# Performance work log

Measured on AMD Instinct MI355X. Metric: run time of the kernel, lower is better.

Reference implementation:

```python
import jax, jax.numpy as jnp
import numpy as np
import math

D_MODEL = 1024
D_HEAD = 64
BATCH = 8
SEQ = 2048


def setup_inputs() -> dict:
    key = jax.random.key(0)
    ks = jax.random.split(key, 5)
    s = 0.02
    return {
        "residual_stream": jax.random.normal(ks[0], (BATCH, SEQ, D_MODEL), dtype=jnp.float32),
        "Wq": jax.random.normal(ks[1], (D_HEAD, D_MODEL), dtype=jnp.float32) * s,
        "Wk": jax.random.normal(ks[2], (D_HEAD, D_MODEL), dtype=jnp.float32) * s,
        "Wv": jax.random.normal(ks[3], (D_HEAD, D_MODEL), dtype=jnp.float32) * s,
        "Wo": jax.random.normal(ks[4], (D_MODEL, D_HEAD), dtype=jnp.float32) * s,
    }


def reference(residual_stream, Wq, Wk, Wv, Wo):
    # NOTE: module scales by 1/sqrt(d_model), NOT 1/sqrt(d_head)
    scale = 1.0 / math.sqrt(D_MODEL)
    q = jnp.einsum('bsd,hd->bsh', residual_stream, Wq)  # [B,S,Dh]
    k = jnp.einsum('bsd,hd->bsh', residual_stream, Wk)  # [B,S,Dh]
    scores = jnp.einsum('bqh,bkh->bqk', q, k) * scale   # [B,S,S]
    seq = scores.shape[-1]
    causal = jnp.tril(jnp.ones((seq, seq), dtype=bool))
    scores = jnp.where(causal[None, :, :], scores, jnp.float32(-jnp.inf))
    attn = jax.nn.softmax(scores, axis=-1)
    # O applied to V *before* the attention-weighted sum (as in the module)
    x = jnp.einsum('bsh,dh->bsd', jnp.einsum('bsd,hd->bsh', residual_stream, Wv), Wo)  # [B,S,Dm]
    return jnp.einsum('bqk,bkd->bqd', attn, x)
```

## Files before the change

kernel.cpp:

```cpp
#include <hip/hip_runtime.h>

#define SEQ 2048
#define DMODEL 1024
#define DHEAD 64
#define NROWS 16384
#define ATT_SC2 0.0450842300667f

typedef __attribute__((ext_vector_type(8))) short bf16x8;
typedef __attribute__((ext_vector_type(4))) float f32x4;
typedef __attribute__((ext_vector_type(4))) unsigned int u32x4;
typedef __attribute__((ext_vector_type(4))) unsigned short u16x4;
typedef __attribute__((ext_vector_type(4))) float fl4;

#define MFMA16(a,b,c) __builtin_amdgcn_mfma_f32_16x16x32_bf16((a),(b),(c),0,0,0)
#define GLL16(g, l) __builtin_amdgcn_global_load_lds( \
    (const __attribute__((address_space(1))) void*)(g), \
    (__attribute__((address_space(3))) void*)(l), 16, 0, 0)

__device__ __forceinline__ unsigned short f2bf(float f) {
    union { float f; unsigned int u; } v; v.f = f;
    unsigned int u = v.u;
    unsigned int r = u + 0x7fffu + ((u >> 16) & 1u);
    return (unsigned short)(r >> 16);
}

__device__ __forceinline__ unsigned int cvtpk(float lo, float hi) {
    unsigned int d;
    asm volatile("v_cvt_pk_bf16_f32 %0, %1, %2" : "=v"(d) : "v"(lo), "v"(hi));
    return d;
}

__global__ __launch_bounds__(256) void k_cvt(
    const float* __restrict__ Wq, const float* __restrict__ Wk,
    const float* __restrict__ Wv, const float* __restrict__ Wo,
    unsigned short* __restrict__ Wb,
    unsigned short* __restrict__ Wob)
{
    int i4 = blockIdx.x * 256 + threadIdx.x;
    const int W1 = 16384;
    const float* src; unsigned short* dst; int off;
    if (i4 < 3 * W1) {
        int which = i4 / W1;
        off = i4 - which * W1;
        src = (which == 0) ? Wq : (which == 1) ? Wk : Wv;
        dst = Wb + (size_t)which * 65536;
    } else {
        off = i4 - 3 * W1; src = Wo; dst = Wob;
    }
    fl4 v = reinterpret_cast<const fl4*>(src)[off];
    u16x4 o;
    o[0] = f2bf(v[0]); o[1] = f2bf(v[1]); o[2] = f2bf(v[2]); o[3] = f2bf(v[3]);
    reinterpret_cast<u16x4*>(dst)[off] = o;
}

__global__ __launch_bounds__(256) void k_qkv(
    const float* __restrict__ x,
    const unsigned short* __restrict__ Wb,
    unsigned short* __restrict__ Qb,
    unsigned short* __restrict__ Kb,
    unsigned short* __restrict__ Vt)
{
    __shared__ __align__(16) char smem[65536];

    int tid = threadIdx.x;
    int wave = tid >> 6, lane = tid & 63, g = lane >> 4, lr = lane & 15;
    int mh = wave & 1, nh = wave >> 1;
    int mbase = blockIdx.x * 32;

    const float* xsrc[2];
#pragma unroll
    for (int j = 0; j < 2; ++j) {
        int ci = j * 256 + tid;
        int row = ci >> 4, c = ci & 15, cg = c ^ (row & 7);
        xsrc[j] = x + (size_t)(mbase + row) * DMODEL + cg * 4;
    }
    const unsigned short* wsrc[6];
#pragma unroll
    for (int j = 0; j < 6; ++j) {
        int ci = (wave * 6 + j) * 64 + lane;
        int row = ci >> 3, c = ci & 7, cg = c ^ (row & 7);
        wsrc[j] = Wb + (size_t)row * DMODEL + cg * 8;
    }

    f32x4 acc[6];
#pragma unroll
    for (int f = 0; f < 6; ++f) acc[f] = (f32x4){0.f, 0.f, 0.f, 0.f};

#pragma unroll
    for (int j = 0; j < 2; ++j) GLL16(xsrc[j], smem + j * 4096 + wave * 1024);
#pragma unroll
    for (int j = 0; j < 6; ++j) GLL16(wsrc[j], smem + 16384 + (wave * 6 + j) * 1024);

    for (int ks = 0; ks < 16; ++ks) {
        int cur = ks & 1;
        if (ks < 15) {
            int nb = cur ^ 1;
#pragma unroll
            for (int j = 0; j < 2; ++j)
                GLL16(xsrc[j] + (ks + 1) * 64, smem + nb * 8192 + j * 4096 + wave * 1024);
#pragma unroll
            for (int j = 0; j < 6; ++j)
                GLL16(wsrc[j] + (ks + 1) * 64,
                      smem + 16384 + nb * 24576 + (wave * 6 + j) * 1024);
            asm volatile("s_waitcnt vmcnt(8)" ::: "memory");
        } else {
            asm volatile("s_waitcnt vmcnt(0)" ::: "memory");
        }
        __builtin_amdgcn_s_barrier();
        asm volatile("" ::: "memory");

        const float* Xf = (const float*)(smem + cur * 8192);
        const unsigned short* Wf = (const unsigned short*)(smem + 16384 + cur * 24576);
        int arow = mh * 16 + lr;
#pragma unroll
        for (int kc = 0; kc < 2; ++kc) {
            int c0 = (kc * 8 + g * 2) ^ (lr & 7);
            int c1 = (kc * 8 + g * 2 + 1) ^ (lr & 7);
            fl4 xa = *(const fl4*)&Xf[arow * 64 + c0 * 4];
            fl4 xb = *(const fl4*)&Xf[arow * 64 + c1 * 4];
            union { unsigned int u[4]; bf16x8 v; } a;
            a.u[0] = cvtpk(xa[0], xa[1]); a.u[1] = cvtpk(xa[2], xa[3]);
            a.u[2] = cvtpk(xb[0], xb[1]); a.u[3] = cvtpk(xb[2], xb[3]);
            __builtin_amdgcn_s_setprio(1);
#pragma unroll
            for (int f = 0; f < 6; ++f) {
                int brow = (nh * 6 + f) * 16 + lr;
                int cb = (kc * 4 + g) ^ (lr & 7);
                bf16x8 b = *(const bf16x8*)&Wf[brow * 64 + cb * 8];
                acc[f] = MFMA16(a.v, b, acc[f]);
            }
            __builtin_amdgcn_s_setprio(0);
        }
        asm volatile("" ::: "memory");
        __builtin_amdgcn_s_barrier();
    }

    unsigned short* tmp = (unsigned short*)smem;
    int mrow = mbase + mh * 16 + g * 4;
#pragma unroll
    for (int f = 0; f < 6; ++f) {
        int fg = nh * 6 + f;
#pragma unroll
        for (int r = 0; r < 4; ++r) {
            unsigned short bv = f2bf(acc[f][r]);
            if (fg < 4)      Qb[(size_t)(mrow + r) * DHEAD + fg * 16 + lr] = bv;
            else if (fg < 8) Kb[(size_t)(mrow + r) * DHEAD + (fg - 4) * 16 + lr] = bv;
            else             tmp[(mh * 16 + g * 4 + r) * 72 + (fg - 8) * 16 + lr] = bv;
        }
    }
    __syncthreads();
    int b = mbase >> 11, sbase = mbase & 2047;
    int h = tid >> 2, sc = tid & 3;
    u32x4 o;
#pragma unroll
    for (int j = 0; j < 4; ++j) {
        o[j] = (unsigned int)tmp[(sc * 8 + 2 * j) * 72 + h] |
               ((unsigned int)tmp[(sc * 8 + 2 * j + 1) * 72 + h] << 16);
    }
    size_t off = ((size_t)(b * 64 + h)) * SEQ + sbase + sc * 8;
    *reinterpret_cast<u32x4*>(&Vt[off]) = o;
}

__global__ __launch_bounds__(256) void k_fused(
    const unsigned short* __restrict__ Qb,
    const unsigned short* __restrict__ Kb,
    const unsigned short* __restrict__ Vt,
    const unsigned short* __restrict__ Wob,
    float* __restrict__ out)
{
    __shared__ __align__(16) char smem[65536];

    int tid = threadIdx.x;
    int wave = tid >> 6, lane = tid & 63, g = lane >> 4, lr = lane & 15;
    int pair = wave >> 1, pw = wave & 1;
    int bid = blockIdx.x;
    int idx = bid & 255;
    int qt = (bid < 256) ? (63 - (idx >> 3)) : (idx >> 3);
    int b = idx & 7;

    const unsigned short* ksrc[2];
    const unsigned short* vsrc[2];
#pragma unroll
    for (int j = 0; j < 2; ++j) {
        int ci = j * 256 + tid;
        int row = ci >> 3, c = ci & 7, cg = c ^ (row & 7);
        ksrc[j] = Kb + ((size_t)(b * SEQ) + row) * DHEAD + cg * 8;
        vsrc[j] = Vt + ((size_t)(b * DHEAD) + row) * SEQ + cg * 8;
    }

#define STAGE(n_, s_) do {                                                   \
    int te_ = (2 * (s_)) * 64;                                               \
    int to_ = ((2 * (s_) + 1 < (n_)) ? (2 * (s_) + 1) : ((n_) - 1)) * 64;    \
    char* base_ = smem + ((s_) & 1) * 32768;                                 \
    _Pragma("unroll")                                                        \
    for (int j_ = 0; j_ < 2; ++j_) {                                         \
        GLL16(ksrc[j_] + (size_t)te_ * DHEAD, base_ + j_ * 4096 + wave * 1024);          \
        GLL16(ksrc[j_] + (size_t)to_ * DHEAD, base_ + 8192 + j_ * 4096 + wave * 1024);   \
        GLL16(vsrc[j_] + te_, base_ + 16384 + j_ * 4096 + wave * 1024);                  \
        GLL16(vsrc[j_] + to_, base_ + 24576 + j_ * 4096 + wave * 1024);                  \
    } } while (0)

    int n = (qt >> 1) + 1;
    int nsteps = (n + 1) >> 1;
    int qw = qt * 32 + pw * 16;
    size_t qrowbase = (size_t)(b * SEQ) + qw;

    bf16x8 aq[2];
#pragma unroll
    for (int kc = 0; kc < 2; ++kc)
        aq[kc] = *(const bf16x8*)&Qb[(qrowbase + lr) * DHEAD + kc * 32 + g * 8];

    STAGE(n, 0);

    float l_part = 0.f;
    f32x4 of[4];
#pragma unroll
    for (int f = 0; f < 4; ++f) of[f] = (f32x4){0.f, 0.f, 0.f, 0.f};

    for (int s = 0; s < nsteps; ++s) {
        if (s + 1 < nsteps) {
            STAGE(n, s + 1);
            asm volatile("s_waitcnt vmcnt(8)" ::: "memory");
        } else {
            asm volatile("s_waitcnt vmcnt(0)" ::: "memory");
        }
        __builtin_amdgcn_s_barrier();
        asm volatile("" ::: "memory");

        int t = 2 * s + pair, kvb = t * 64;
        if (t < n && kvb <= qw + 15) {
            const unsigned short* Kl =
                (const unsigned short*)(smem + (s & 1) * 32768 + pair * 8192);
            const unsigned short* Vl =
                (const unsigned short*)(smem + (s & 1) * 32768 + 16384 + pair * 8192);

            f32x4 s4[4];
#pragma unroll
            for (int f = 0; f < 4; ++f) s4[f] = (f32x4){0.f, 0.f, 0.f, 0.f};
            __builtin_amdgcn_s_setprio(1);
#pragma unroll
            for (int kc = 0; kc < 2; ++kc) {
#pragma unroll
                for (int f = 0; f < 4; ++f) {
                    int brow = f * 16 + lr;
                    int cb = (kc * 4 + g) ^ (lr & 7);
                    bf16x8 bk = *(const bf16x8*)&Kl[brow * 64 + cb * 8];
                    s4[f] = MFMA16(bk, aq[kc], s4[f]);
                }
            }
            __builtin_amdgcn_s_setprio(0);

            if (kvb + 63 <= qw) {
#pragma unroll
                for (int f = 0; f < 4; ++f)
#pragma unroll
                    for (int r = 0; r < 4; ++r) {
                        float p = exp2f(s4[f][r] * ATT_SC2);
                        s4[f][r] = p;
                        l_part += p;
                    }
            } else {
                int qr = qw + lr;
#pragma unroll
                for (int f = 0; f < 4; ++f) {
#pragma unroll
                    for (int r = 0; r < 4; ++r) {
                        int kvg = kvb + f * 16 + g * 4 + r;
                        float p = exp2f(s4[f][r] * ATT_SC2);
                        p = (kvg > qr) ? 0.f : p;
                        s4[f][r] = p;
                        l_part += p;
                    }
                }
            }
            unsigned int pk[4][2];
#pragma unroll
            for (int f = 0; f < 4; ++f) {
                pk[f][0] = cvtpk(s4[f][0], s4[f][1]);
                pk[f][1] = cvtpk(s4[f][2], s4[f][3]);
            }
#pragma unroll
            for (int kc = 0; kc < 2; ++kc) {
                unsigned int A = pk[2 * kc][0],     Bv = pk[2 * kc][1];
                unsigned int C = pk[2 * kc + 1][0], D  = pk[2 * kc + 1][1];
                asm("v_permlane32_swap_b32 %0, %1" : "+v"(A), "+v"(C));
                asm("v_permlane16_swap_b32 %0, %1" : "+v"(A), "+v"(C));
                asm("v_permlane32_swap_b32 %0, %1" : "+v"(Bv), "+v"(D));
                asm("v_permlane16_swap_b32 %0, %1" : "+v"(Bv), "+v"(D));
                union { unsigned int u[4]; bf16x8 v; } ap;
                ap.u[0] = A; ap.u[1] = Bv; ap.u[2] = C; ap.u[3] = D;
                __builtin_amdgcn_s_setprio(1);
#pragma unroll
                for (int fd = 0; fd < 4; ++fd) {
                    int vrow = fd * 16 + lr;
                    int cv = (kc * 4 + g) ^ (lr & 7);
                    bf16x8 bv = *(const bf16x8*)&Vl[vrow * 64 + cv * 8];
                    of[fd] = MFMA16(ap.v, bv, of[fd]);
                }
                __builtin_amdgcn_s_setprio(0);
            }
        }
        asm volatile("" ::: "memory");
        __builtin_amdgcn_s_barrier();
    }

    {
        float* Obuf = (float*)(smem + pair * 8704);
        float* Ol = (float*)(smem + 17408);
        float ls = l_part;
        ls += __shfl_xor(ls, 16);
        ls += __shfl_xor(ls, 32);
        if (lane < 16) Ol[pair * 32 + pw * 16 + lane] = ls;
        int row32 = pw * 16 + g * 4;
#pragma unroll
        for (int r = 0; r < 4; ++r)
#pragma unroll
            for (int fd = 0; fd < 4; ++fd)
                Obuf[(row32 + r) * 68 + fd * 16 + lr] = of[fd][r];
    }
    __syncthreads();

    bf16x8 ao[2][2];
    {
        const float* O0 = (const float*)smem;
        const float* O1 = (const float*)(smem + 8704);
        const float* Ol = (const float*)(smem + 17408);
#pragma unroll
        for (int m = 0; m < 2; ++m) {
            int arow = m * 16 + lr;
            float inv = 1.f / (Ol[arow] + Ol[32 + arow]);
#pragma unroll
            for (int kc = 0; kc < 2; ++kc) {
                int cb = arow * 68 + kc * 32 + g * 8;
                fl4 xa = *(const fl4*)&O0[cb], xb = *(const fl4*)&O0[cb + 4];
                fl4 ya = *(const fl4*)&O1[cb], yb = *(const fl4*)&O1[cb + 4];
                union { unsigned int u[4]; bf16x8 v; } a;
                a.u[0] = cvtpk((xa[0] + ya[0]) * inv, (xa[1] + ya[1]) * inv);
                a.u[1] = cvtpk((xa[2] + ya[2]) * inv, (xa[3] + ya[3]) * inv);
                a.u[2] = cvtpk((xb[0] + yb[0]) * inv, (xb[1] + yb[1]) * inv);
                a.u[3] = cvtpk((xb[2] + yb[2]) * inv, (xb[3] + yb[3]) * inv);
                ao[m][kc] = a.v;
            }
        }
    }

    {
        int nb = wave * 256;
        f32x4 acc[2][16];
#pragma unroll
        for (int m = 0; m < 2; ++m)
#pragma unroll
            for (int f = 0; f < 16; ++f) acc[m][f] = (f32x4){0.f, 0.f, 0.f, 0.f};
#pragma unroll
        for (int kc = 0; kc < 2; ++kc) {
            __builtin_amdgcn_s_setprio(1);
#pragma unroll
            for (int f = 0; f < 16; ++f) {
                bf16x8 bw = *(const bf16x8*)
                    &Wob[(size_t)(nb + f * 16 + lr) * DHEAD + kc * 32 + g * 8];
                acc[0][f] = MFMA16(ao[0][kc], bw, acc[0][f]);
                acc[1][f] = MFMA16(ao[1][kc], bw, acc[1][f]);
            }
            __builtin_amdgcn_s_setprio(0);
        }
        int mb = b * SEQ + qt * 32;
#pragma unroll
        for (int m = 0; m < 2; ++m) {
            int mrow = mb + m * 16 + g * 4;
#pragma unroll
            for (int f = 0; f < 16; ++f)
#pragma unroll
                for (int r = 0; r < 4; ++r)
                    out[(size_t)(mrow + r) * DMODEL + nb + f * 16 + lr] = acc[m][f][r];
        }
    }
#undef STAGE
}

extern "C" void kernel_launch(void* const* d_in, const int* in_sizes, int n_in,
                              void* d_out, int out_size, void* d_ws, size_t ws_size,
                              hipStream_t stream) {
    const float* x  = (const float*)d_in[0];
    const float* Wq = (const float*)d_in[1];
    const float* Wk = (const float*)d_in[2];
    const float* Wv = (const float*)d_in[3];
    const float* Wo = (const float*)d_in[4];
    float* out = (float*)d_out;

    unsigned short* Wb  = (unsigned short*)d_ws;
    unsigned short* Wob = Wb + 196608;
    unsigned short* Qb  = Wob + 65536;
    unsigned short* Kb  = Qb + 1048576;
    unsigned short* Vt  = Kb + 1048576;

    k_cvt<<<256, 256, 0, stream>>>(Wq, Wk, Wv, Wo, Wb, Wob);
    k_qkv<<<512, 256, 0, stream>>>(x, Wb, Qb, Kb, Vt);
    k_fused<<<512, 256, 0, stream>>>(Qb, Kb, Vt, Wob, out);
}
```

Baseline: 55.40 us.

## Simplify attention kernel to 2 waves reading K/V directly from global

```diff
diff --git a/kernel.cpp b/kernel.cpp
--- a/kernel.cpp
+++ b/kernel.cpp
@@ -161,220 +161,143 @@
     *reinterpret_cast<u32x4*>(&Vt[off]) = o;
 }
 
-__global__ __launch_bounds__(256) void k_fused(
+__global__ __launch_bounds__(128) void k_fused(
     const unsigned short* __restrict__ Qb,
     const unsigned short* __restrict__ Kb,
     const unsigned short* __restrict__ Vt,
     const unsigned short* __restrict__ Wob,
     float* __restrict__ out)
 {
-    __shared__ __align__(16) char smem[65536];
+    __shared__ __align__(16) float Obuf[2][16 * 68];
+
+    const f32x4 zero4 = {0.f, 0.f, 0.f, 0.f};
 
     int tid = threadIdx.x;
     int wave = tid >> 6, lane = tid & 63, g = lane >> 4, lr = lane & 15;
-    int pair = wave >> 1, pw = wave & 1;
     int bid = blockIdx.x;
     int idx = bid & 255;
     int qt = (bid < 256) ? (63 - (idx >> 3)) : (idx >> 3);
     int b = idx & 7;
-
-    const unsigned short* ksrc[2];
-    const unsigned short* vsrc[2];
-#pragma unroll
-    for (int j = 0; j < 2; ++j) {
-        int ci = j * 256 + tid;
-        int row = ci >> 3, c = ci & 7, cg = c ^ (row & 7);
-        ksrc[j] = Kb + ((size_t)(b * SEQ) + row) * DHEAD + cg * 8;
-        vsrc[j] = Vt + ((size_t)(b * DHEAD) + row) * SEQ + cg * 8;
-    }
-
-#define STAGE(n_, s_) do {                                                   \
-    int te_ = (2 * (s_)) * 64;                                               \
-    int to_ = ((2 * (s_) + 1 < (n_)) ? (2 * (s_) + 1) : ((n_) - 1)) * 64;    \
-    char* base_ = smem + ((s_) & 1) * 32768;                                 \
-    _Pragma("unroll")                                                        \
-    for (int j_ = 0; j_ < 2; ++j_) {                                         \
-        GLL16(ksrc[j_] + (size_t)te_ * DHEAD, base_ + j_ * 4096 + wave * 1024);          \
-        GLL16(ksrc[j_] + (size_t)to_ * DHEAD, base_ + 8192 + j_ * 4096 + wave * 1024);   \
-        GLL16(vsrc[j_] + te_, base_ + 16384 + j_ * 4096 + wave * 1024);                  \
-        GLL16(vsrc[j_] + to_, base_ + 24576 + j_ * 4096 + wave * 1024);                  \
-    } } while (0)
-
-    int n = (qt >> 1) + 1;
-    int nsteps = (n + 1) >> 1;
-    int qw = qt * 32 + pw * 16;
+    int qw = qt * 32 + wave * 16;
     size_t qrowbase = (size_t)(b * SEQ) + qw;
+
+    const unsigned short* Kbase = Kb + (size_t)(b * SEQ) * DHEAD;
+    const unsigned short* Vbase = Vt + (size_t)(b * DHEAD) * SEQ;
 
     bf16x8 aq[2];
 #pragma unroll
     for (int kc = 0; kc < 2; ++kc)
         aq[kc] = *(const bf16x8*)&Qb[(qrowbase + lr) * DHEAD + kc * 32 + g * 8];
 
-    STAGE(n, 0);
+    int n = (qw >> 6) + 1;
 
     float l_part = 0.f;
     f32x4 of[4];
 #pragma unroll
-    for (int f = 0; f < 4; ++f) of[f] = (f32x4){0.f, 0.f, 0.f, 0.f};
-
-    for (int s = 0; s < nsteps; ++s) {
-        if (s + 1 < nsteps) {
-            STAGE(n, s + 1);
-            asm volatile("s_waitcnt vmcnt(8)" ::: "memory");
+    for (int f = 0; f < 4; ++f) of[f] = zero4;
+
+    for (int t = 0; t < n; ++t) {
+        int kvb = t * 64;
+
+        f32x4 s4[4];
+#pragma unroll
+        for (int f = 0; f < 4; ++f) s4[f] = zero4;
+#pragma unroll
+        for (int kc = 0; kc < 2; ++kc) {
+#pragma unroll
+            for (int f = 0; f < 4; ++f) {
+                bf16x8 bk = *(const bf16x8*)
+                    &Kbase[(size_t)(kvb + f * 16 + lr) * DHEAD + kc * 32 + g * 8];
+                s4[f] = MFMA16(bk, aq[kc], s4[f]);
+            }
+        }
+
+        if (kvb + 63 <= qw) {
+#pragma unroll
+            for (int f = 0; f < 4; ++f)
+#pragma unroll
+                for (int r = 0; r < 4; ++r) {
+                    float p = exp2f(s4[f][r] * ATT_SC2);
+                    s4[f][r] = p;
+                    l_part += p;
+                }
         } else {
-            asm volatile("s_waitcnt vmcnt(0)" ::: "memory");
-        }
-        __builtin_amdgcn_s_barrier();
-        asm volatile("" ::: "memory");
-
-        int t = 2 * s + pair, kvb = t * 64;
-        if (t < n && kvb <= qw + 15) {
-            const unsigned short* Kl =
-                (const unsigned short*)(smem + (s & 1) * 32768 + pair * 8192);
-            const unsigned short* Vl =
-                (const unsigned short*)(smem + (s & 1) * 32768 + 16384 + pair * 8192);
-
-            f32x4 s4[4];
-#pragma unroll
-            for (int f = 0; f < 4; ++f) s4[f] = (f32x4){0.f, 0.f, 0.f, 0.f};
-            __builtin_amdgcn_s_setprio(1);
-#pragma unroll
-            for (int kc = 0; kc < 2; ++kc) {
-#pragma unroll
-                for (int f = 0; f < 4; ++f) {
-                    int brow = f * 16 + lr;
-                    int cb = (kc * 4 + g) ^ (lr & 7);
-                    bf16x8 bk = *(const bf16x8*)&Kl[brow * 64 + cb * 8];
-                    s4[f] = MFMA16(bk, aq[kc], s4[f]);
+            int qr = qw + lr;
+#pragma unroll
+            for (int f = 0; f < 4; ++f) {
+#pragma unroll
+                for (int r = 0; r < 4; ++r) {
+                    int kvg = kvb + f * 16 + g * 4 + r;
+                    float p = exp2f(s4[f][r] * ATT_SC2);
+                    p = (kvg > qr) ? 0.f : p;
+                    s4[f][r] = p;
+                    l_part += p;
                 }
             }
-            __builtin_amdgcn_s_setprio(0);
-
-            if (kvb + 63 <= qw) {
-#pragma unroll
-                for (int f = 0; f < 4; ++f)
-#pragma unroll
-                    for (int r = 0; r < 4; ++r) {
-                        float p = exp2f(s4[f][r] * ATT_SC2);
-                        s4[f][r] = p;
-                        l_part += p;
-                    }
-            } else {
-                int qr = qw + lr;
-#pragma unroll
-                for (int f = 0; f < 4; ++f) {
-#pragma unroll
-                    for (int r = 0; r < 4; ++r) {
-                        int kvg = kvb + f * 16 + g * 4 + r;
-                        float p = exp2f(s4[f][r] * ATT_SC2);
-                        p = (kvg > qr) ? 0.f : p;
-                        s4[f][r] = p;
-                        l_part += p;
-                    }
-                }
+        }
+        unsigned int pk[4][2];
+#pragma unroll
+        for (int f = 0; f < 4; ++f) {
+            pk[f][0] = cvtpk(s4[f][0], s4[f][1]);
+            pk[f][1] = cvtpk(s4[f][2], s4[f][3]);
+        }
+#pragma unroll
+        for (int kc = 0; kc < 2; ++kc) {
+            unsigned int A = pk[2 * kc][0],     Bv = pk[2 * kc][1];
+            unsigned int C = pk[2 * kc + 1][0], D  = pk[2 * kc + 1][1];
+            asm("v_permlane32_swap_b32 %0, %1" : "+v"(A), "+v"(C));
+            asm("v_permlane16_swap_b32 %0, %1" : "+v"(A), "+v"(C));
+            asm("v_permlane32_swap_b32 %0, %1" : "+v"(Bv), "+v"(D));
+            asm("v_permlane16_swap_b32 %0, %1" : "+v"(Bv), "+v"(D));
+            union { unsigned int u[4]; bf16x8 v; } ap;
+            ap.u[0] = A; ap.u[1] = Bv; ap.u[2] = C; ap.u[3] = D;
+#pragma unroll
+            for (int fd = 0; fd < 4; ++fd) {
+                bf16x8 bv = *(const bf16x8*)
+                    &Vbase[(size_t)(fd * 16 + lr) * SEQ + kvb + kc * 32 + g * 8];
+                of[fd] = MFMA16(ap.v, bv, of[fd]);
             }
-            unsigned int pk[4][2];
-#pragma unroll
-            for (int f = 0; f < 4; ++f) {
-                pk[f][0] = cvtpk(s4[f][0], s4[f][1]);
-                pk[f][1] = cvtpk(s4[f][2], s4[f][3]);
-            }
-#pragma unroll
-            for (int kc = 0; kc < 2; ++kc) {
-                unsigned int A = pk[2 * kc][0],     Bv = pk[2 * kc][1];
-                unsigned int C = pk[2 * kc + 1][0], D  = pk[2 * kc + 1][1];
-                asm("v_permlane32_swap_b32 %0, %1" : "+v"(A), "+v"(C));
-                asm("v_permlane16_swap_b32 %0, %1" : "+v"(A), "+v"(C));
-                asm("v_permlane32_swap_b32 %0, %1" : "+v"(Bv), "+v"(D));
-                asm("v_permlane16_swap_b32 %0, %1" : "+v"(Bv), "+v"(D));
-                union { unsigned int u[4]; bf16x8 v; } ap;
-                ap.u[0] = A; ap.u[1] = Bv; ap.u[2] = C; ap.u[3] = D;
-                __builtin_amdgcn_s_setprio(1);
-#pragma unroll
-                for (int fd = 0; fd < 4; ++fd) {
-                    int vrow = fd * 16 + lr;
-                    int cv = (kc * 4 + g) ^ (lr & 7);
-                    bf16x8 bv = *(const bf16x8*)&Vl[vrow * 64 + cv * 8];
-                    of[fd] = MFMA16(ap.v, bv, of[fd]);
-                }
-                __builtin_amdgcn_s_setprio(0);
-            }
-        }
-        asm volatile("" ::: "memory");
-        __builtin_amdgcn_s_barrier();
-    }
-
-    {
-        float* Obuf = (float*)(smem + pair * 8704);
-        float* Ol = (float*)(smem + 17408);
-        float ls = l_part;
-        ls += __shfl_xor(ls, 16);
-        ls += __shfl_xor(ls, 32);
-        if (lane < 16) Ol[pair * 32 + pw * 16 + lane] = ls;
-        int row32 = pw * 16 + g * 4;
+        }
+    }
+
+    float ls = l_part;
+    ls += __shfl_xor(ls, 16);
+    ls += __shfl_xor(ls, 32);
+    float inv = 1.0f / ls;
+
+    float* ob = Obuf[wave];
+#pragma unroll
+    for (int fd = 0; fd < 4; ++fd)
 #pragma unroll
         for (int r = 0; r < 4; ++r)
-#pragma unroll
-            for (int fd = 0; fd < 4; ++fd)
-                Obuf[(row32 + r) * 68 + fd * 16 + lr] = of[fd][r];
-    }
-    __syncthreads();
-
-    bf16x8 ao[2][2];
-    {
-        const float* O0 = (const float*)smem;
-        const float* O1 = (const float*)(smem + 8704);
-        const float* Ol = (const float*)(smem + 17408);
-#pragma unroll
-        for (int m = 0; m < 2; ++m) {
-            int arow = m * 16 + lr;
-            float inv = 1.f / (Ol[arow] + Ol[32 + arow]);
-#pragma unroll
-            for (int kc = 0; kc < 2; ++kc) {
-                int cb = arow * 68 + kc * 32 + g * 8;
-                fl4 xa = *(const fl4*)&O0[cb], xb = *(const fl4*)&O0[cb + 4];
-                fl4 ya = *(const fl4*)&O1[cb], yb = *(const fl4*)&O1[cb + 4];
-                union { unsigned int u[4]; bf16x8 v; } a;
-                a.u[0] = cvtpk((xa[0] + ya[0]) * inv, (xa[1] + ya[1]) * inv);
-                a.u[1] = cvtpk((xa[2] + ya[2]) * inv, (xa[3] + ya[3]) * inv);
-                a.u[2] = cvtpk((xb[0] + yb[0]) * inv, (xb[1] + yb[1]) * inv);
-                a.u[3] = cvtpk((xb[2] + yb[2]) * inv, (xb[3] + yb[3]) * inv);
-                ao[m][kc] = a.v;
-            }
-        }
-    }
-
-    {
-        int nb = wave * 256;
-        f32x4 acc[2][16];
-#pragma unroll
-        for (int m = 0; m < 2; ++m)
-#pragma unroll
-            for (int f = 0; f < 16; ++f) acc[m][f] = (f32x4){0.f, 0.f, 0.f, 0.f};
-#pragma unroll
-        for (int kc = 0; kc < 2; ++kc) {
-            __builtin_amdgcn_s_setprio(1);
-#pragma unroll
-            for (int f = 0; f < 16; ++f) {
-                bf16x8 bw = *(const bf16x8*)
-                    &Wob[(size_t)(nb + f * 16 + lr) * DHEAD + kc * 32 + g * 8];
-                acc[0][f] = MFMA16(ao[0][kc], bw, acc[0][f]);
-                acc[1][f] = MFMA16(ao[1][kc], bw, acc[1][f]);
-            }
-            __builtin_amdgcn_s_setprio(0);
-        }
-        int mb = b * SEQ + qt * 32;
-#pragma unroll
-        for (int m = 0; m < 2; ++m) {
-            int mrow = mb + m * 16 + g * 4;
-#pragma unroll
-            for (int f = 0; f < 16; ++f)
-#pragma unroll
-                for (int r = 0; r < 4; ++r)
-                    out[(size_t)(mrow + r) * DMODEL + nb + f * 16 + lr] = acc[m][f][r];
-        }
-    }
-#undef STAGE
+            ob[(g * 4 + r) * 68 + fd * 16 + lr] = of[fd][r];
+
+    bf16x8 ao[2];
+#pragma unroll
+    for (int kc = 0; kc < 2; ++kc) {
+        fl4 xa = *(const fl4*)&ob[lr * 68 + kc * 32 + g * 8];
+        fl4 xb = *(const fl4*)&ob[lr * 68 + kc * 32 + g * 8 + 4];
+        union { unsigned int u[4]; bf16x8 v; } a;
+        a.u[0] = cvtpk(xa[0] * inv, xa[1] * inv);
+        a.u[1] = cvtpk(xa[2] * inv, xa[3] * inv);
+        a.u[2] = cvtpk(xb[0] * inv, xb[1] * inv);
+        a.u[3] = cvtpk(xb[2] * inv, xb[3] * inv);
+        ao[kc] = a.v;
+    }
+
+    float* orow = out + qrowbase * DMODEL;
+#pragma unroll 2
+    for (int nc = 0; nc < 4; ++nc) {
+#pragma unroll
+        for (int f = 0; f < 16; ++f) {
+            int n0 = nc * 256 + f * 16;
+            bf16x8 bw0 = *(const bf16x8*)&Wob[(size_t)(n0 + lr) * DHEAD + g * 8];
+            bf16x8 bw1 = *(const bf16x8*)&Wob[(size_t)(n0 + lr) * DHEAD + 32 + g * 8];
+            f32x4 acc = MFMA16(bw0, ao[0], zero4);
+            acc = MFMA16(bw1, ao[1], acc);
+            *(fl4*)&orow[(size_t)lr * DMODEL + n0 + g * 4] = acc;
+        }
+    }
 }
 
 extern "C" void kernel_launch(void* const* d_in, const int* in_sizes, int n_in,
@@ -395,5 +318,5 @@
 
     k_cvt<<<256, 256, 0, stream>>>(Wq, Wk, Wv, Wo, Wb, Wob);
     k_qkv<<<512, 256, 0, stream>>>(x, Wb, Qb, Kb, Vt);
-    k_fused<<<512, 256, 0, stream>>>(Qb, Kb, Vt, Wob, out);
-}
+    k_fused<<<512, 128, 0, stream>>>(Qb, Kb, Vt, Wob, out);
+}
```

Result: slower. 95.52 us (+72.4%).
